# Kernel tuning notes

Measured on AMD Instinct MI355X. Metric: run time of the kernel, lower is better.

The kernel has to match this reference:

```python
import jax, jax.numpy as jnp
import numpy as np

DIM = 1024
SEQ_LEN = 4096
K_RANK = 256
HEADS = 16
HEAD_DIM = DIM // HEADS
BATCH = 4


def setup_inputs() -> dict:
    key = jax.random.key(0)
    k1, k2, k3, k4 = jax.random.split(key, 4)
    x = jax.random.normal(k1, (BATCH, SEQ_LEN, DIM), dtype=jnp.float32)
    W_qkv = jax.random.normal(k2, (DIM, 3 * DIM), dtype=jnp.float32) * (DIM ** -0.5)
    E = jax.random.normal(k3, (SEQ_LEN, K_RANK), dtype=jnp.float32)
    W_out = jax.random.normal(k4, (DIM, DIM), dtype=jnp.float32) * (DIM ** -0.5)
    b_out = jnp.zeros((DIM,), dtype=jnp.float32)
    return {"x": x, "W_qkv": W_qkv, "E": E, "W_out": W_out, "b_out": b_out}


def reference(x, W_qkv, E, W_out, b_out):
    B, N, D = x.shape
    scale = HEAD_DIM ** -0.5
    qkv = x @ W_qkv                                    # [B, N, 3D]
    q, k, v = jnp.split(qkv, 3, axis=-1)
    # [B, N, D] -> [B, H, N, hd]
    reshape_heads = lambda t: t.reshape(B, N, HEADS, HEAD_DIM).transpose(0, 2, 1, 3)
    q, k, v = map(reshape_heads, (q, k, v))
    # Linformer low-rank projection along sequence: [B, H, N, hd] -> [B, H, k, hd]
    k_proj = jnp.einsum('bhnd,nk->bhkd', k, E)
    v_proj = jnp.einsum('bhnd,nk->bhkd', v, E)
    scores = jnp.einsum('bhnd,bhkd->bhnk', q, k_proj) * scale  # [B, H, N, k]
    attn = jax.nn.softmax(scores, axis=-1)
    out = jnp.einsum('bhnk,bhkd->bhnd', attn, v_proj)  # [B, H, N, hd]
    out = out.transpose(0, 2, 1, 3).reshape(B, N, D)
    return out @ W_out + b_out
```

## Files before the change

kernel.cpp:

```cpp
#include <hip/hip_runtime.h>
#include <hip/hip_bf16.h>

typedef _Float16 f16;
typedef __attribute__((ext_vector_type(4))) _Float16 f16x4;
typedef __attribute__((ext_vector_type(8))) _Float16 f16x8;
typedef __attribute__((ext_vector_type(4))) float f32x4;

#define DIM 1024
#define SEQ 4096
#define KRNK 256
#define NH 16
#define HD 64
#define NB 4
#define ROWS (NB*SEQ)
#define NSPLIT 4

typedef const void __attribute__((address_space(1))) as1cv;
typedef void __attribute__((address_space(3))) as3v;

static __device__ __forceinline__ void glds16(const void* g, void* l) {
  __builtin_amdgcn_global_load_lds((as1cv*)g, (as3v*)l, 16, 0, 0);
}

template<int MODE>
__global__ __launch_bounds__(256) void k_prep_w(const float* __restrict__ in,
                                                f16* __restrict__ oh, f16* __restrict__ ol,
                                                int R, int C) {
  __shared__ float tile[64][65];
  int rtiles = R >> 6;
  int rt = blockIdx.x % rtiles, ct = blockIdx.x / rtiles;
  int r0 = rt << 6, c0 = ct << 6, t = threadIdx.x;
#pragma unroll
  for (int i = 0; i < 16; ++i) {
    int e = t + i * 256; int r = e >> 6, c = e & 63;
    tile[r][c] = in[(size_t)(r0 + r) * C + c0 + c];
  }
  __syncthreads();
#pragma unroll
  for (int i = 0; i < 16; ++i) {
    int e = t + i * 256; int c = e >> 6, r = e & 63;
    float v = tile[r][c];
    size_t idx = (size_t)(c0 + c) * R + r0 + r;
    if constexpr (MODE == 0) {
      v *= 256.0f;
      f16 h = (f16)v;
      oh[idx] = h;
      ol[idx] = (f16)(v - (float)h);
    } else {
      oh[idx] = (f16)v;
    }
  }
}

template<bool WH>
__global__ __launch_bounds__(256) void k_tsplit(const float* __restrict__ in,
                                                f16* __restrict__ oh,
                                                f16* __restrict__ oth,
                                                int R, int C) {
  __shared__ float tile[64][65];
  int rtiles = R >> 6;
  int rt = blockIdx.x % rtiles, ct = blockIdx.x / rtiles;
  int r0 = rt << 6, c0 = ct << 6, t = threadIdx.x;
  int cq = (t & 15) * 4, rr = t >> 4;
#pragma unroll
  for (int i = 0; i < 4; ++i) {
    int r = rr + i * 16;
    f32x4 v = *(const f32x4*)&in[(size_t)(r0 + r) * C + c0 + cq];
    tile[r][cq] = v[0]; tile[r][cq + 1] = v[1];
    tile[r][cq + 2] = v[2]; tile[r][cq + 3] = v[3];
    if constexpr (WH) {
      f16x4 h = {(f16)v[0], (f16)v[1], (f16)v[2], (f16)v[3]};
      *(f16x4*)&oh[(size_t)(r0 + r) * C + c0 + cq] = h;
    }
  }
  __syncthreads();
  int d4 = (t >> 4) * 4, sq = (t & 15) * 4;
#pragma unroll
  for (int j = 0; j < 4; ++j) {
    f16x4 h4;
#pragma unroll
    for (int k = 0; k < 4; ++k) h4[k] = (f16)tile[sq + k][d4 + j];
    *(f16x4*)&oth[(size_t)(c0 + d4 + j) * R + r0 + sq] = h4;
  }
}

template<bool ASPL, bool BSPL, int MT, int NT>
static __device__ __forceinline__ void mm_core(
    const f16* __restrict__ Ah, const f16* __restrict__ Al, int lda,
    const f16* __restrict__ Bh, const f16* __restrict__ Bl, int ldb,
    int bm, int bn, int K,
    f16* sAh, f16* sAl, f16* sBh, f16* sBl,
    f32x4 (&acc)[MT / 32][NT / 32]) {
  constexpr int MREP = MT / 32, NREP = NT / 32;
  constexpr int AI = MT / 32, BI = NT / 32;
  const int t = threadIdx.x;
  const int lane = t & 63, w = t >> 6;
  const int wr = w >> 1, wc = w & 1;
  const int l15 = lane & 15, hi = lane >> 4;
  const f32x4 zero = {0.f, 0.f, 0.f, 0.f};
#pragma unroll
  for (int m = 0; m < MREP; ++m)
#pragma unroll
    for (int n = 0; n < NREP; ++n) acc[m][n] = zero;

  for (int kk = 0; kk < K; kk += 64) {
#pragma unroll
    for (int i = 0; i < AI; ++i) {
      int c = t + i * 256;
      int row = c >> 3, cc = c & 7;
      size_t g = (size_t)(bm + row) * lda + kk + cc * 8;
      glds16(Ah + g, &sAh[c * 8]);
      if constexpr (ASPL) glds16(Al + g, &sAl[c * 8]);
    }
#pragma unroll
    for (int i = 0; i < BI; ++i) {
      int c = t + i * 256;
      int row = c >> 3, cc = c & 7;
      size_t g = (size_t)(bn + row) * ldb + kk + cc * 8;
      glds16(Bh + g, &sBh[c * 8]);
      if constexpr (BSPL) glds16(Bl + g, &sBl[c * 8]);
    }
    __syncthreads();

    f16x8 avh[MREP][2], avl[MREP][2], bvh[NREP][2], bvl[NREP][2];
#pragma unroll
    for (int m = 0; m < MREP; ++m)
#pragma unroll
      for (int ks = 0; ks < 2; ++ks) {
        int off = (wr * (MT / 2) + m * 16 + l15) * 64 + ks * 32 + hi * 8;
        avh[m][ks] = *(const f16x8*)&sAh[off];
        if constexpr (ASPL) avl[m][ks] = *(const f16x8*)&sAl[off];
      }
#pragma unroll
    for (int n = 0; n < NREP; ++n)
#pragma unroll
      for (int ks = 0; ks < 2; ++ks) {
        int off = (wc * (NT / 2) + n * 16 + l15) * 64 + ks * 32 + hi * 8;
        bvh[n][ks] = *(const f16x8*)&sBh[off];
        if constexpr (BSPL) bvl[n][ks] = *(const f16x8*)&sBl[off];
      }
#pragma unroll
    for (int m = 0; m < MREP; ++m)
#pragma unroll
      for (int n = 0; n < NREP; ++n)
#pragma unroll
        for (int ks = 0; ks < 2; ++ks) {
          if constexpr (ASPL && BSPL) {
            acc[m][n] = __builtin_amdgcn_mfma_f32_16x16x32_f16(avl[m][ks], bvh[n][ks], acc[m][n], 0, 0, 0);
            acc[m][n] = __builtin_amdgcn_mfma_f32_16x16x32_f16(avh[m][ks], bvl[n][ks], acc[m][n], 0, 0, 0);
          } else if constexpr (BSPL) {
            acc[m][n] = __builtin_amdgcn_mfma_f32_16x16x32_f16(avh[m][ks], bvl[n][ks], acc[m][n], 0, 0, 0);
          }
          acc[m][n] = __builtin_amdgcn_mfma_f32_16x16x32_f16(avh[m][ks], bvh[n][ks], acc[m][n], 0, 0, 0);
        }
    __syncthreads();
  }
}

__global__ __launch_bounds__(256) void k_xe2(const f16* __restrict__ Eth,
                                             const f16* __restrict__ xth,
                                             float* __restrict__ XEp) {
  __shared__ __align__(16) f16 sA[128 * 64];
  __shared__ __align__(16) f16 sB[64 * 64];
  int bx = blockIdx.x;
  int nt = bx & 15, mt = (bx >> 4) & 1, b = (bx >> 5) & 3, sp = bx >> 7;
  int bm = mt << 7, bn = nt << 6;
  int koff = sp * (SEQ / NSPLIT);
  f32x4 acc[4][2];
  mm_core<false, false, 128, 64>(Eth + koff, nullptr, SEQ,
                                 xth + (size_t)b * SEQ + koff, nullptr, ROWS,
                                 bm, bn, SEQ / NSPLIT, sA, nullptr, sB, nullptr, acc);
  const int t = threadIdx.x, lane = t & 63, w = t >> 6;
  const int wr = w >> 1, wc = w & 1, l15 = lane & 15, hi = lane >> 4;
#pragma unroll
  for (int m = 0; m < 4; ++m)
#pragma unroll
    for (int n = 0; n < 2; ++n)
#pragma unroll
      for (int r = 0; r < 4; ++r) {
        int kr = bm + wr * 64 + m * 16 + hi * 4 + r;
        int dd = bn + wc * 32 + n * 16 + l15;
        XEp[(((size_t)sp * NB + b) * KRNK + kr) * DIM + dd] = acc[m][n][r];
      }
}

__global__ __launch_bounds__(256) void k_xered(const float* __restrict__ XEp,
                                               f16* __restrict__ XEh,
                                               f16* __restrict__ XEl) {
  size_t i = (size_t)blockIdx.x * 256 + threadIdx.x;
  const size_t sstride = (size_t)NB * KRNK * DIM / 4;
  const f32x4* p = (const f32x4*)XEp;
  f32x4 s = p[i];
#pragma unroll
  for (int sp = 1; sp < NSPLIT; ++sp) s += p[i + sp * sstride];
  f16x4 h4, l4;
#pragma unroll
  for (int j = 0; j < 4; ++j) {
    f16 h = (f16)s[j];
    h4[j] = h;
    l4[j] = (f16)(s[j] - (float)h);
  }
  *(f16x4*)&XEh[i * 4] = h4;
  *(f16x4*)&XEl[i * 4] = l4;
}

__global__ __launch_bounds__(256) void k_gq(const f16* __restrict__ xh,
                                            const f16* __restrict__ Wph,
                                            f16* __restrict__ q) {
  __shared__ __align__(16) f16 sA[64 * 64];
  __shared__ __align__(16) f16 sB[128 * 64];
  int bx = blockIdx.x;
  int mt = bx & 255, nt = bx >> 8;
  int bm = mt << 6, bn = nt << 7;
  f32x4 acc[2][4];
  mm_core<false, false, 64, 128>(xh, nullptr, DIM, Wph, nullptr, DIM, bm, bn, DIM,
                                 sA, nullptr, sB, nullptr, acc);
  const int t = threadIdx.x, lane = t & 63, w = t >> 6;
  const int wr = w >> 1, wc = w & 1, l15 = lane & 15, hi = lane >> 4;
#pragma unroll
  for (int m = 0; m < 2; ++m)
#pragma unroll
    for (int n = 0; n < 4; ++n)
#pragma unroll
      for (int r = 0; r < 4; ++r) {
        int row = bm + wr * 32 + m * 16 + hi * 4 + r;
        int col = bn + wc * 64 + n * 16 + l15;
        q[(size_t)row * DIM + col] = (f16)(acc[m][n][r] * (1.0f / 256.0f));
      }
}

__global__ __launch_bounds__(256) void k_t2(const f16* __restrict__ XEh,
                                            const f16* __restrict__ XEl,
                                            const f16* __restrict__ Wph,
                                            const f16* __restrict__ Wpl,
                                            f16* __restrict__ kph,
                                            f16* __restrict__ vpt) {
  __shared__ __align__(16) f16 sAh[128 * 64], sAl[128 * 64];
  __shared__ __align__(16) f16 sBh[64 * 64], sBl[64 * 64];
  int bx = blockIdx.x;
  int nt = bx & 15, mt = (bx >> 4) & 1, b = (bx >> 5) & 3, kv = bx >> 7;
  size_t abase = (size_t)b * KRNK * DIM;
  size_t wbase = (size_t)(DIM + kv * DIM) * DIM;
  f32x4 acc[4][2];
  mm_core<true, true, 128, 64>(XEh + abase, XEl + abase, DIM, Wph + wbase, Wpl + wbase, DIM,
                               mt << 7, nt << 6, DIM, sAh, sAl, sBh, sBl, acc);
  const int t = threadIdx.x, lane = t & 63, w = t >> 6;
  const int wr = w >> 1, wc = w & 1, l15 = lane & 15, hi = lane >> 4;
#pragma unroll
  for (int m = 0; m < 4; ++m)
#pragma unroll
    for (int n = 0; n < 2; ++n)
#pragma unroll
      for (int r = 0; r < 4; ++r) {
        int row = (mt << 7) + wr * 64 + m * 16 + hi * 4 + r;
        int col = (nt << 6) + wc * 32 + n * 16 + l15;
        float s = acc[m][n][r] * (1.0f / 256.0f);
        if (!kv) kph[((size_t)(b * KRNK + row)) * DIM + col] = (f16)s;
        else     vpt[((size_t)(b * DIM + col)) * KRNK + row] = (f16)s;
      }
}

__global__ __launch_bounds__(256) void k_attn(const f16* __restrict__ q,
                                              const f16* __restrict__ kph,
                                              const f16* __restrict__ vpt,
                                              f16* __restrict__ oattn) {
  __shared__ __align__(16) f16 sBuf[2][64 * 64];
  __shared__ __align__(16) f16 sP[64 * KRNK];
  int bx0 = blockIdx.x;
  int swz = (bx0 & 7) * 512 + (bx0 >> 3);
  int qb = swz & 63;
  int bh = swz >> 6;
  int b = bh >> 4, h = bh & 15;
  int t = threadIdx.x;
  int lane = t & 63, w = t >> 6;
  int l15 = lane & 15, hi = lane >> 4;

  const f16* kbase = kph + ((size_t)(b * KRNK)) * DIM + h * HD;
  const f16* vbase = vpt + ((size_t)(b * DIM + h * HD)) * KRNK;

  auto stageK = [&](int c, int bufi) {
#pragma unroll
    for (int i = 0; i < 2; ++i) {
      int sid = w * 128 + i * 64 + lane;
      int kr = sid >> 3, sl = sid & 7;
      glds16(kbase + (size_t)(c * 64 + kr) * DIM + ((sl ^ (kr & 7)) * 8),
             &sBuf[bufi][sid * 8]);
    }
  };
  auto stageV = [&](int c, int bufi) {
#pragma unroll
    for (int i = 0; i < 2; ++i) {
      int sid = w * 128 + i * 64 + lane;
      int hd = sid >> 3, sl = sid & 7;
      glds16(vbase + (size_t)hd * KRNK + c * 64 + ((sl ^ (hd & 7)) * 8),
             &sBuf[bufi][sid * 8]);
    }
  };

  int seqrow = qb * 64 + w * 16 + l15;
  const f16* qg = q + ((size_t)(b * SEQ + seqrow)) * DIM + h * HD;
  f16x8 aq[2];
  aq[0] = *(const f16x8*)(qg + hi * 8);
  aq[1] = *(const f16x8*)(qg + 32 + hi * 8);

  const f32x4 zero = {0.f, 0.f, 0.f, 0.f};
  f32x4 s[16];

  stageK(0, 0);
#pragma unroll
  for (int c = 0; c < 4; ++c) {
    __syncthreads();
    if (c < 3) stageK(c + 1, (c + 1) & 1);
    else       stageV(0, 0);
#pragma unroll
    for (int n = 0; n < 4; ++n) {
      int nn = c * 4 + n;
      s[nn] = zero;
      int krl = n * 16 + l15;
#pragma unroll
      for (int ks = 0; ks < 2; ++ks) {
        f16x8 bk = *(const f16x8*)&sBuf[c & 1][krl * 64 + (((ks * 4 + hi) ^ (krl & 7)) * 8)];
        s[nn] = __builtin_amdgcn_mfma_f32_16x16x32_f16(aq[ks], bk, s[nn], 0, 0, 0);
      }
    }
  }

  const float scale = 0.125f;
  float mx[4], sminv[4];
#pragma unroll
  for (int r = 0; r < 4; ++r) {
    float m0 = s[0][r];
#pragma unroll
    for (int n = 1; n < 16; ++n) m0 = fmaxf(m0, s[n][r]);
#pragma unroll
    for (int d = 1; d <= 8; d <<= 1) m0 = fmaxf(m0, __shfl_xor(m0, d));
    mx[r] = m0;
  }
  float sm[4] = {0.f, 0.f, 0.f, 0.f};
#pragma unroll
  for (int n = 0; n < 16; ++n)
#pragma unroll
    for (int r = 0; r < 4; ++r) {
      float p = __expf((s[n][r] - mx[r]) * scale);
      s[n][r] = p;
      sm[r] += p;
    }
#pragma unroll
  for (int r = 0; r < 4; ++r) {
    float t2 = sm[r];
#pragma unroll
    for (int d = 1; d <= 8; d <<= 1) t2 += __shfl_xor(t2, d);
    sminv[r] = 1.0f / t2;
  }

#pragma unroll
  for (int n = 0; n < 16; ++n)
#pragma unroll
    for (int r = 0; r < 4; ++r) {
      int qloc = w * 16 + hi * 4 + r;
      int kr = n * 16 + l15;
      int chunk = kr >> 3;
      sP[qloc * KRNK + ((chunk ^ (qloc & 7)) * 8) + (kr & 7)] = (f16)s[n][r];
    }

  f32x4 o[4];
#pragma unroll
  for (int n = 0; n < 4; ++n) o[n] = zero;
  int qloc = w * 16 + l15;
#pragma unroll
  for (int c = 0; c < 4; ++c) {
    __syncthreads();
    if (c < 3) stageV(c + 1, (c + 1) & 1);
#pragma unroll
    for (int sub = 0; sub < 2; ++sub) {
      int chunk = c * 8 + sub * 4 + hi;
      f16x8 pa = *(const f16x8*)&sP[qloc * KRNK + ((chunk ^ (qloc & 7)) * 8)];
#pragma unroll
      for (int n = 0; n < 4; ++n) {
        int hd = n * 16 + l15;
        f16x8 bv = *(const f16x8*)&sBuf[c & 1][hd * 64 + (((sub * 4 + hi) ^ (hd & 7)) * 8)];
        o[n] = __builtin_amdgcn_mfma_f32_16x16x32_f16(pa, bv, o[n], 0, 0, 0);
      }
    }
  }

  size_t obase = ((size_t)(b * SEQ + qb * 64)) * DIM + h * HD;
#pragma unroll
  for (int n = 0; n < 4; ++n)
#pragma unroll
    for (int r = 0; r < 4; ++r) {
      int qloc2 = w * 16 + hi * 4 + r;
      int hd = n * 16 + l15;
      oattn[obase + (size_t)qloc2 * DIM + hd] = (f16)(o[n][r] * sminv[r]);
    }
}

__global__ __launch_bounds__(256) void k_go(const f16* __restrict__ oattn,
                                            const f16* __restrict__ WoT,
                                            const float* __restrict__ bias,
                                            float* __restrict__ out) {
  __shared__ __align__(16) f16 sA[64 * 64];
  __shared__ __align__(16) f16 sB[128 * 64];
  int bx = blockIdx.x;
  int mt = bx & 255, nt = bx >> 8;
  int bm = mt << 6, bn = nt << 7;
  f32x4 acc[2][4];
  mm_core<false, false, 64, 128>(oattn, nullptr, DIM, WoT, nullptr, DIM, bm, bn, DIM,
                                 sA, nullptr, sB, nullptr, acc);
  const int t = threadIdx.x, lane = t & 63, w = t >> 6;
  const int wr = w >> 1, wc = w & 1, l15 = lane & 15, hi = lane >> 4;
#pragma unroll
  for (int m = 0; m < 2; ++m)
#pragma unroll
    for (int n = 0; n < 4; ++n)
#pragma unroll
      for (int r = 0; r < 4; ++r) {
        int row = bm + wr * 32 + m * 16 + hi * 4 + r;
        int col = bn + wc * 64 + n * 16 + l15;
        out[(size_t)row * DIM + col] = acc[m][n][r] + bias[col];
      }
}

extern "C" void kernel_launch(void* const* d_in, const int* in_sizes, int n_in,
                              void* d_out, int out_size, void* d_ws, size_t ws_size,
                              hipStream_t stream) {
  const float* x    = (const float*)d_in[0];
  const float* Wqkv = (const float*)d_in[1];
  const float* E    = (const float*)d_in[2];
  const float* Wout = (const float*)d_in[3];
  const float* bout = (const float*)d_in[4];
  float* out = (float*)d_out;

  char* p = (char*)d_ws;
  f16* Wph = (f16*)p;  p += (size_t)2 * 3 * DIM * DIM;
  f16* Wpl = (f16*)p;  p += (size_t)2 * 3 * DIM * DIM;
  f16* WoT = (f16*)p;  p += (size_t)2 * DIM * DIM;
  f16* xh  = (f16*)p;  p += (size_t)2 * ROWS * DIM;
  f16* xth = (f16*)p;  p += (size_t)2 * DIM * ROWS;
  f16* Eth = (f16*)p;  p += (size_t)2 * KRNK * SEQ;
  f16* XEh = (f16*)p;  p += (size_t)2 * NB * KRNK * DIM;
  f16* XEl = (f16*)p;  p += (size_t)2 * NB * KRNK * DIM;
  f16* kph = (f16*)p;  p += (size_t)2 * NB * KRNK * DIM;
  f16* vpt = (f16*)p;  p += (size_t)2 * NB * DIM * KRNK;
  f16* oattn = (f16*)p; p += (size_t)2 * ROWS * DIM;
  float* XEp = (float*)p;  p += (size_t)4 * NSPLIT * NB * KRNK * DIM;
  size_t need = (size_t)(p - (char*)d_ws);
  if (ws_size < need) return;

  f16* q = xth;

  k_prep_w<0><<<(DIM / 64) * (3 * DIM / 64), 256, 0, stream>>>(Wqkv, Wph, Wpl, DIM, 3 * DIM);
  k_prep_w<1><<<(DIM / 64) * (DIM / 64), 256, 0, stream>>>(Wout, WoT, nullptr, DIM, DIM);
  k_tsplit<true><<<(ROWS / 64) * (DIM / 64), 256, 0, stream>>>(x, xh, xth, ROWS, DIM);
  k_tsplit<false><<<(SEQ / 64) * (KRNK / 64), 256, 0, stream>>>(E, nullptr, Eth, SEQ, KRNK);
  k_xe2<<<512, 256, 0, stream>>>(Eth, xth, XEp);
  k_xered<<<(NB * KRNK * DIM / 4) / 256, 256, 0, stream>>>(XEp, XEh, XEl);
  k_gq<<<2048, 256, 0, stream>>>(xh, Wph, q);
  k_t2<<<256, 256, 0, stream>>>(XEh, XEl, Wph, Wpl, kph, vpt);
  k_attn<<<64 * 64, 256, 0, stream>>>(q, kph, vpt, oattn);
  k_go<<<2048, 256, 0, stream>>>(oattn, WoT, bout, out);
}
```

Measured before the change: 261.5 us.

## Double-buffer GEMM LDS tiles and remap blocks for XCD-local L2 reuse

The shared GEMM core now uses two LDS buffers and issues the global-to-LDS loads for the next K slice before computing the current one. This removes one barrier per iteration and overlaps memory latency with MFMA work. The q and output-projection GEMMs also get a block-index remap that gives each XCD a contiguous range of row tiles, improving L2 locality. The cost is double the LDS per block, which may reduce occupancy, especially in the split-precision kernel.

```diff
diff --git a/kernel.cpp b/kernel.cpp
--- a/kernel.cpp
+++ b/kernel.cpp
@@ -93,6 +93,7 @@
     f32x4 (&acc)[MT / 32][NT / 32]) {
   constexpr int MREP = MT / 32, NREP = NT / 32;
   constexpr int AI = MT / 32, BI = NT / 32;
+  constexpr int ASZ = MT * 64, BSZ = NT * 64;
   const int t = threadIdx.x;
   const int lane = t & 63, w = t >> 6;
   const int wr = w >> 1, wc = w & 1;
@@ -103,31 +104,37 @@
 #pragma unroll
     for (int n = 0; n < NREP; ++n) acc[m][n] = zero;
 
-  for (int kk = 0; kk < K; kk += 64) {
+  auto stage = [&](int kk, int bufi) {
 #pragma unroll
     for (int i = 0; i < AI; ++i) {
       int c = t + i * 256;
       int row = c >> 3, cc = c & 7;
       size_t g = (size_t)(bm + row) * lda + kk + cc * 8;
-      glds16(Ah + g, &sAh[c * 8]);
-      if constexpr (ASPL) glds16(Al + g, &sAl[c * 8]);
+      glds16(Ah + g, &sAh[bufi * ASZ + c * 8]);
+      if constexpr (ASPL) glds16(Al + g, &sAl[bufi * ASZ + c * 8]);
     }
 #pragma unroll
     for (int i = 0; i < BI; ++i) {
       int c = t + i * 256;
       int row = c >> 3, cc = c & 7;
       size_t g = (size_t)(bn + row) * ldb + kk + cc * 8;
-      glds16(Bh + g, &sBh[c * 8]);
-      if constexpr (BSPL) glds16(Bl + g, &sBl[c * 8]);
-    }
+      glds16(Bh + g, &sBh[bufi * BSZ + c * 8]);
+      if constexpr (BSPL) glds16(Bl + g, &sBl[bufi * BSZ + c * 8]);
+    }
+  };
+
+  stage(0, 0);
+  int cur = 0;
+  for (int kk = 0; kk < K; kk += 64) {
     __syncthreads();
+    if (kk + 64 < K) stage(kk + 64, cur ^ 1);
 
     f16x8 avh[MREP][2], avl[MREP][2], bvh[NREP][2], bvl[NREP][2];
 #pragma unroll
     for (int m = 0; m < MREP; ++m)
 #pragma unroll
       for (int ks = 0; ks < 2; ++ks) {
-        int off = (wr * (MT / 2) + m * 16 + l15) * 64 + ks * 32 + hi * 8;
+        int off = cur * ASZ + (wr * (MT / 2) + m * 16 + l15) * 64 + ks * 32 + hi * 8;
         avh[m][ks] = *(const f16x8*)&sAh[off];
         if constexpr (ASPL) avl[m][ks] = *(const f16x8*)&sAl[off];
       }
@@ -135,7 +142,7 @@
     for (int n = 0; n < NREP; ++n)
 #pragma unroll
       for (int ks = 0; ks < 2; ++ks) {
-        int off = (wc * (NT / 2) + n * 16 + l15) * 64 + ks * 32 + hi * 8;
+        int off = cur * BSZ + (wc * (NT / 2) + n * 16 + l15) * 64 + ks * 32 + hi * 8;
         bvh[n][ks] = *(const f16x8*)&sBh[off];
         if constexpr (BSPL) bvl[n][ks] = *(const f16x8*)&sBl[off];
       }
@@ -153,15 +160,15 @@
           }
           acc[m][n] = __builtin_amdgcn_mfma_f32_16x16x32_f16(avh[m][ks], bvh[n][ks], acc[m][n], 0, 0, 0);
         }
-    __syncthreads();
+    cur ^= 1;
   }
 }
 
 __global__ __launch_bounds__(256) void k_xe2(const f16* __restrict__ Eth,
                                              const f16* __restrict__ xth,
                                              float* __restrict__ XEp) {
-  __shared__ __align__(16) f16 sA[128 * 64];
-  __shared__ __align__(16) f16 sB[64 * 64];
+  __shared__ __align__(16) f16 sA[2 * 128 * 64];
+  __shared__ __align__(16) f16 sB[2 * 64 * 64];
   int bx = blockIdx.x;
   int nt = bx & 15, mt = (bx >> 4) & 1, b = (bx >> 5) & 3, sp = bx >> 7;
   int bm = mt << 7, bn = nt << 6;
@@ -204,14 +211,20 @@
   *(f16x4*)&XEl[i * 4] = l4;
 }
 
+static __device__ __forceinline__ void go_map(int bx, int& bm, int& bn) {
+  int xcd = bx & 7, idx = bx >> 3;
+  int nt = idx & 7, mt = xcd * 32 + (idx >> 3);
+  bm = mt << 6;
+  bn = nt << 7;
+}
+
 __global__ __launch_bounds__(256) void k_gq(const f16* __restrict__ xh,
                                             const f16* __restrict__ Wph,
                                             f16* __restrict__ q) {
-  __shared__ __align__(16) f16 sA[64 * 64];
-  __shared__ __align__(16) f16 sB[128 * 64];
-  int bx = blockIdx.x;
-  int mt = bx & 255, nt = bx >> 8;
-  int bm = mt << 6, bn = nt << 7;
+  __shared__ __align__(16) f16 sA[2 * 64 * 64];
+  __shared__ __align__(16) f16 sB[2 * 128 * 64];
+  int bm, bn;
+  go_map(blockIdx.x, bm, bn);
   f32x4 acc[2][4];
   mm_core<false, false, 64, 128>(xh, nullptr, DIM, Wph, nullptr, DIM, bm, bn, DIM,
                                  sA, nullptr, sB, nullptr, acc);
@@ -235,8 +248,8 @@
                                             const f16* __restrict__ Wpl,
                                             f16* __restrict__ kph,
                                             f16* __restrict__ vpt) {
-  __shared__ __align__(16) f16 sAh[128 * 64], sAl[128 * 64];
-  __shared__ __align__(16) f16 sBh[64 * 64], sBl[64 * 64];
+  __shared__ __align__(16) f16 sAh[2 * 128 * 64], sAl[2 * 128 * 64];
+  __shared__ __align__(16) f16 sBh[2 * 64 * 64], sBl[2 * 64 * 64];
   int bx = blockIdx.x;
   int nt = bx & 15, mt = (bx >> 4) & 1, b = (bx >> 5) & 3, kv = bx >> 7;
   size_t abase = (size_t)b * KRNK * DIM;
@@ -399,11 +412,10 @@
                                             const f16* __restrict__ WoT,
                                             const float* __restrict__ bias,
                                             float* __restrict__ out) {
-  __shared__ __align__(16) f16 sA[64 * 64];
-  __shared__ __align__(16) f16 sB[128 * 64];
-  int bx = blockIdx.x;
-  int mt = bx & 255, nt = bx >> 8;
-  int bm = mt << 6, bn = nt << 7;
+  __shared__ __align__(16) f16 sA[2 * 64 * 64];
+  __shared__ __align__(16) f16 sB[2 * 128 * 64];
+  int bm, bn;
+  go_map(blockIdx.x, bm, bn);
   f32x4 acc[2][4];
   mm_core<false, false, 64, 128>(oattn, nullptr, DIM, WoT, nullptr, DIM, bm, bn, DIM,
                                  sA, nullptr, sB, nullptr, acc);
```

Result: no change. 263.6 us (+0.8%).
